# Performance work log

Measured on AMD Instinct MI355X. Metric: run time of the kernel, lower is better.

## Reference

```python
import jax, jax.numpy as jnp
import numpy as np


def setup_inputs() -> dict:
    key = jax.random.key(0)
    ks = jax.random.split(key, 6)
    Q, S, D, C = 128, 512, 768, 64
    return {
        "query_reps": jax.random.normal(ks[0], (Q, D), dtype=jnp.float32),
        "support_reps": jax.random.normal(ks[1], (S, D), dtype=jnp.float32),
        "W1": jax.random.normal(ks[2], (2 * D, 2 * D), dtype=jnp.float32) * 0.02,
        "b1": jnp.zeros((2 * D,), dtype=jnp.float32),
        "W2": jax.random.normal(ks[3], (1, 2 * D), dtype=jnp.float32) * 0.02,
        "b2": jnp.zeros((1,), dtype=jnp.float32),
        "support_labels": jnp.sort(jax.random.randint(ks[4], (S,), 0, C)),
        "query_target_ids": jax.random.randint(ks[5], (Q,), 0, C),
        "num_classes": C,
    }


def reference(query_reps, support_reps, W1, b1, W2, b2,
              support_labels, query_target_ids, num_classes):
    D = query_reps.shape[1]
    # Original: concat_reps = cat([repeat_interleave(q, S), s.repeat(Q)], dim=1)
    # then relu(Linear_2Dx2D(concat)). Equivalent split-weight form avoids the
    # explicit [Q*S, 2D] concat: x @ W1.T = q @ W1[:, :D].T + s @ W1[:, D:].T
    hq = query_reps @ W1[:, :D].T        # [Q, 2D]
    hs = support_reps @ W1[:, D:].T      # [S, 2D]
    h = jax.nn.relu(hq[:, None, :] + hs[None, :, :] + b1)   # [Q, S, 2D]
    scores = jnp.einsum('qsd,d->qs', h, W2[0]) + b2[0]       # [Q, S]
    # aggregate_scores_by_label with support_reduction='score':
    # M one-hot [C, S] row-normalized (p=1) => per-label mean of scores.
    seg = jax.ops.segment_sum(scores.T, support_labels,
                              num_segments=num_classes).T     # [Q, C]
    counts = jax.ops.segment_sum(jnp.ones((support_labels.shape[0],), jnp.float32),
                                 support_labels, num_segments=num_classes)
    agg = seg / jnp.maximum(counts, 1.0)                      # [Q, C]
    logp = jax.nn.log_softmax(agg, axis=1)
    loss = -jnp.mean(jnp.take_along_axis(logp, query_target_ids[:, None], axis=1))
    preds = jnp.argmax(agg, axis=1)
    return (loss, preds == query_target_ids)
```

## Files before the change

kernel.cpp:

```cpp
#include <hip/hip_runtime.h>
#include <math.h>

#define QN 128
#define SN 512
#define DN 768
#define TDN 1536
#define CN 64
#define KSPLIT 2
#define KCH 384

#define HQP_ELEMS (KSPLIT * QN * TDN)
#define HSP_ELEMS (KSPLIT * SN * TDN)
#define ZERO_ELEMS (QN * CN)

typedef short short8 __attribute__((ext_vector_type(8)));
typedef float f32x4 __attribute__((ext_vector_type(4)));

#define LDS_STRIDE 40
#define PLANE (128 * LDS_STRIDE)

__device__ __forceinline__ short bf16_rtn(float x) {
    unsigned u = __float_as_uint(x);
    return (short)((u + 0x7fffu + ((u >> 16) & 1u)) >> 16);
}
__device__ __forceinline__ float bf16_tof(short s) {
    return __uint_as_float(((unsigned)(unsigned short)s) << 16);
}

__global__ __launch_bounds__(256) void gemm_kernel(
    const float* __restrict__ query, const float* __restrict__ support,
    const float* __restrict__ W1, float* __restrict__ hqp, float* __restrict__ hsp,
    float* __restrict__ zbuf, int* __restrict__ donecnt)
{
    const int nt = blockIdx.x;
    const int mt = blockIdx.y;
    const int kz = blockIdx.z;
    const int tid = threadIdx.x;

    if (nt == 0 && kz == 0) {
        int o = (mt * 256 + tid) * 8;
        if (o < ZERO_ELEMS) {
            *(float4*)&zbuf[o]     = make_float4(0.f, 0.f, 0.f, 0.f);
            *(float4*)&zbuf[o + 4] = make_float4(0.f, 0.f, 0.f, 0.f);
        }
        if (mt == 0 && tid == 0) *donecnt = 0;
    }

    const float* A;
    float* Cout;
    int M0, Koff;
    if (mt == 0) { A = query;   M0 = 0;              Koff = 0;  Cout = hqp + (size_t)kz * QN * TDN; }
    else         { A = support; M0 = (mt - 1) * 128; Koff = DN; Cout = hsp + (size_t)kz * SN * TDN; }

    __shared__ short lds[2][4][PLANE];

    const int r  = tid >> 1;
    const int kh = (tid & 1) * 16;

    const float* Arow = &A [(size_t)(M0 + r) * DN  + kz * KCH + kh];
    const float* Brow = &W1[(size_t)(nt * 128 + r) * TDN + Koff + kz * KCH + kh];

    f32x4 acc[4][4];
    #pragma unroll
    for (int i = 0; i < 4; ++i)
        #pragma unroll
        for (int j = 0; j < 4; ++j)
            acc[i][j] = (f32x4){0.f, 0.f, 0.f, 0.f};

    auto stage = [&](short* plane, float4 v0, float4 v1, float4 v2, float4 v3) {
        float f[16] = {v0.x,v0.y,v0.z,v0.w, v1.x,v1.y,v1.z,v1.w,
                       v2.x,v2.y,v2.z,v2.w, v3.x,v3.y,v3.z,v3.w};
        short hi[16], lo[16];
        #pragma unroll
        for (int i = 0; i < 16; ++i) {
            hi[i] = bf16_rtn(f[i]);
            lo[i] = bf16_rtn(f[i] - bf16_tof(hi[i]));
        }
        short* dsth = plane + r * LDS_STRIDE + kh;
        #pragma unroll
        for (int i = 0; i < 16; ++i) dsth[i] = hi[i];
        short* dstl = plane + PLANE + r * LDS_STRIDE + kh;
        #pragma unroll
        for (int i = 0; i < 16; ++i) dstl[i] = lo[i];
    };

    {
        float4 a0 = *(const float4*)(Arow),     a1 = *(const float4*)(Arow + 4);
        float4 a2 = *(const float4*)(Arow + 8), a3 = *(const float4*)(Arow + 12);
        float4 b0 = *(const float4*)(Brow),     b1 = *(const float4*)(Brow + 4);
        float4 b2 = *(const float4*)(Brow + 8), b3 = *(const float4*)(Brow + 12);
        stage(lds[0][0], a0, a1, a2, a3);
        stage(lds[0][2], b0, b1, b2, b3);
    }
    __syncthreads();

    const int lane  = tid & 63;
    const int w     = tid >> 6;
    const int lm    = lane & 15;
    const int quad  = lane >> 4;
    const int wrow0 = (w >> 1) * 64;
    const int wcol0 = (w & 1) * 64;

    int buf = 0;
    for (int step = 0; step < 12; ++step) {
        float4 a0, a1, a2, a3, b0, b1, b2, b3;
        if (step < 11) {
            const float* An = Arow + (step + 1) * 32;
            const float* Bn = Brow + (step + 1) * 32;
            a0 = *(const float4*)(An);     a1 = *(const float4*)(An + 4);
            a2 = *(const float4*)(An + 8); a3 = *(const float4*)(An + 12);
            b0 = *(const float4*)(Bn);     b1 = *(const float4*)(Bn + 4);
            b2 = *(const float4*)(Bn + 8); b3 = *(const float4*)(Bn + 12);
        }

        const short* Ah = lds[buf][0];
        const short* Al = lds[buf][1];
        const short* Bh = lds[buf][2];
        const short* Bl = lds[buf][3];

        short8 ah[4], al[4], bh[4], bl[4];
        #pragma unroll
        for (int mi = 0; mi < 4; ++mi) {
            int off = (wrow0 + mi * 16 + lm) * LDS_STRIDE + quad * 8;
            ah[mi] = *(const short8*)&Ah[off];
            al[mi] = *(const short8*)&Al[off];
        }
        #pragma unroll
        for (int ni = 0; ni < 4; ++ni) {
            int off = (wcol0 + ni * 16 + lm) * LDS_STRIDE + quad * 8;
            bh[ni] = *(const short8*)&Bh[off];
            bl[ni] = *(const short8*)&Bl[off];
        }
        #pragma unroll
        for (int mi = 0; mi < 4; ++mi)
            #pragma unroll
            for (int ni = 0; ni < 4; ++ni) {
                acc[mi][ni] = __builtin_amdgcn_mfma_f32_16x16x32_bf16(ah[mi], bh[ni], acc[mi][ni], 0, 0, 0);
                acc[mi][ni] = __builtin_amdgcn_mfma_f32_16x16x32_bf16(ah[mi], bl[ni], acc[mi][ni], 0, 0, 0);
                acc[mi][ni] = __builtin_amdgcn_mfma_f32_16x16x32_bf16(al[mi], bh[ni], acc[mi][ni], 0, 0, 0);
            }

        if (step < 11) {
            int nb = buf ^ 1;
            stage(lds[nb][0], a0, a1, a2, a3);
            stage(lds[nb][2], b0, b1, b2, b3);
            __syncthreads();
            buf = nb;
        }
    }

    #pragma unroll
    for (int mi = 0; mi < 4; ++mi)
        #pragma unroll
        for (int ni = 0; ni < 4; ++ni) {
            int grow = M0 + wrow0 + mi * 16 + quad * 4;
            int gcol = nt * 128 + wcol0 + ni * 16 + lm;
            #pragma unroll
            for (int rr = 0; rr < 4; ++rr)
                Cout[(size_t)(grow + rr) * TDN + gcol] = acc[mi][ni][rr];
        }
}

__global__ __launch_bounds__(256) void score_kernel(
    const float* __restrict__ hqp, const float* __restrict__ hsp,
    const float* __restrict__ b1, const float* __restrict__ W2,
    const int* __restrict__ labels, const int* __restrict__ tgt,
    float* __restrict__ aggbuf, int* __restrict__ donecnt,
    float* __restrict__ out)
{
    const int jc = blockIdx.x;
    const int qt = blockIdx.y;
    const int st = blockIdx.z;

    __shared__ float hqT[96][64];
    __shared__ float hsT[96][64];
    __shared__ float w2s[96];
    __shared__ float sc[64][68];
    __shared__ int   lab[64];
    __shared__ float cnt[CN];
    __shared__ float red[2];
    __shared__ int   isLast;

    const int tid = threadIdx.x;
    if (tid < 64) lab[tid] = labels[st * 64 + tid];

    #pragma unroll
    for (int l = 0; l < 6; ++l) {
        int idx  = tid + l * 256;
        int row  = idx / 24;
        int quad = idx - row * 24;
        int j    = jc * 96 + quad * 4;
        float4 hv = *(const float4*)&b1[j];
        float4 sv = make_float4(0.f, 0.f, 0.f, 0.f);
        #pragma unroll
        for (int p = 0; p < KSPLIT; ++p) {
            float4 h = *(const float4*)&hqp[(size_t)p * QN * TDN + (size_t)(qt * 64 + row) * TDN + j];
            float4 g = *(const float4*)&hsp[(size_t)p * SN * TDN + (size_t)(st * 64 + row) * TDN + j];
            hv.x += h.x; hv.y += h.y; hv.z += h.z; hv.w += h.w;
            sv.x += g.x; sv.y += g.y; sv.z += g.z; sv.w += g.w;
        }
        hqT[quad*4+0][row] = hv.x; hqT[quad*4+1][row] = hv.y;
        hqT[quad*4+2][row] = hv.z; hqT[quad*4+3][row] = hv.w;
        hsT[quad*4+0][row] = sv.x; hsT[quad*4+1][row] = sv.y;
        hsT[quad*4+2][row] = sv.z; hsT[quad*4+3][row] = sv.w;
    }
    if (tid < 24) {
        float4 wv = *(const float4*)&W2[jc * 96 + tid * 4];
        w2s[tid*4+0] = wv.x; w2s[tid*4+1] = wv.y;
        w2s[tid*4+2] = wv.z; w2s[tid*4+3] = wv.w;
    }
    __syncthreads();

    const int tx = tid & 15;
    const int ty = tid >> 4;
    float acc[4][4];
    #pragma unroll
    for (int i = 0; i < 4; ++i)
        #pragma unroll
        for (int j = 0; j < 4; ++j) acc[i][j] = 0.0f;

    #pragma unroll 4
    for (int jj = 0; jj < 96; ++jj) {
        float4 a4 = *(const float4*)&hqT[jj][ty * 4];
        float4 b4 = *(const float4*)&hsT[jj][tx * 4];
        float wv = w2s[jj];
        float a[4] = {a4.x, a4.y, a4.z, a4.w};
        float b[4] = {b4.x, b4.y, b4.z, b4.w};
        #pragma unroll
        for (int i = 0; i < 4; ++i)
            #pragma unroll
            for (int j = 0; j < 4; ++j)
                acc[i][j] += wv * fmaxf(a[i] + b[j], 0.0f);
    }

    #pragma unroll
    for (int i = 0; i < 4; ++i)
        *(float4*)&sc[ty * 4 + i][tx * 4] =
            make_float4(acc[i][0], acc[i][1], acc[i][2], acc[i][3]);
    __syncthreads();

    {
        int row = tid >> 2;
        int seg = tid & 3;
        float* aggrow = aggbuf + (size_t)(qt * 64 + row) * CN;
        int   runc = lab[seg * 16];
        float runv = 0.0f;
        #pragma unroll
        for (int k = 0; k < 16; ++k) {
            int s = seg * 16 + k;
            int c = lab[s];
            if (c != runc) { atomicAdd(&aggrow[runc], runv); runv = 0.0f; runc = c; }
            runv += sc[row][s];
        }
        atomicAdd(&aggrow[runc], runv);
    }

    __syncthreads();
    if (tid == 0) {
        __threadfence();
        isLast = (atomicAdd(donecnt, 1) == 255);
    }
    __syncthreads();
    if (!isLast) return;
    __threadfence();

    if (tid < CN) cnt[tid] = 0.0f;
    __syncthreads();
    atomicAdd(&cnt[labels[tid]],       1.0f);
    atomicAdd(&cnt[labels[tid + 256]], 1.0f);
    __syncthreads();

    float lossv = 0.0f;
    if (tid < QN) {
        const int q = tid;
        const float* rowp = aggbuf + (size_t)q * CN;
        const int t = tgt[q];
        float best = -1e30f, vt = 0.0f;
        int bi = 0;
        #pragma unroll
        for (int c = 0; c < CN; ++c) {
            float v = __hip_atomic_load(&rowp[c], __ATOMIC_RELAXED,
                                        __HIP_MEMORY_SCOPE_AGENT)
                      / fmaxf(cnt[c], 1.0f);
            if (v > best) { best = v; bi = c; }
            if (c == t) vt = v;
        }
        float e = 0.0f;
        #pragma unroll
        for (int c = 0; c < CN; ++c) {
            float v = __hip_atomic_load(&rowp[c], __ATOMIC_RELAXED,
                                        __HIP_MEMORY_SCOPE_AGENT)
                      / fmaxf(cnt[c], 1.0f);
            e += expf(v - best);
        }
        out[1 + q] = (bi == t) ? 1.0f : 0.0f;
        lossv = -(vt - best - logf(e));
    }
    #pragma unroll
    for (int off = 1; off < 64; off <<= 1)
        lossv += __shfl_xor(lossv, off);
    if ((tid & 63) == 0) red[tid >> 6] = lossv;
    __syncthreads();
    if (tid == 0) out[0] = (red[0] + red[1]) / (float)QN;
}

extern "C" void kernel_launch(void* const* d_in, const int* in_sizes, int n_in,
                              void* d_out, int out_size, void* d_ws, size_t ws_size,
                              hipStream_t stream) {
    const float* query   = (const float*)d_in[0];
    const float* support = (const float*)d_in[1];
    const float* W1      = (const float*)d_in[2];
    const float* b1      = (const float*)d_in[3];
    const float* W2      = (const float*)d_in[4];
    const int* labels = (const int*)d_in[6];
    const int* tgt    = (const int*)d_in[7];

    float* ws      = (float*)d_ws;
    float* hqp     = ws;
    float* hsp     = hqp + HQP_ELEMS;
    float* aggbuf  = hsp + HSP_ELEMS;
    int*   donecnt = (int*)(aggbuf + QN * CN);
    float* out     = (float*)d_out;

    hipLaunchKernelGGL(gemm_kernel, dim3(12, 5, 2), dim3(256), 0, stream,
                       query, support, W1, hqp, hsp, aggbuf, donecnt);
    hipLaunchKernelGGL(score_kernel, dim3(16, 2, 8), dim3(256), 0, stream,
                       hqp, hsp, b1, W2, labels, tgt, aggbuf, donecnt, out);
}
```

Measured before the change: 143.6 us.

## Halve score-kernel D chunk, swizzle LDS row-major tiles, atomics from registers

The score kernel's hidden-dimension chunk drops from 96 to 48, doubling the grid to 512 blocks to raise parallelism across CUs. Staged hq/hs tiles are now stored row-major with an XOR swizzle and read as float4 per row, replacing the transposed scalar LDS stores. The score tile no longer goes through shared memory: each thread does the label-run segmented atomicAdds directly from its register accumulators. The trade-off is more global atomics, since each thread now issues at least one per row per block, plus twice the blocks contending on the completion counter.

```diff
diff --git a/kernel.cpp b/kernel.cpp
--- a/kernel.cpp
+++ b/kernel.cpp
@@ -161,6 +161,9 @@
         }
 }
 
+#define JC 48
+#define SSTR 68
+
 __global__ __launch_bounds__(256) void score_kernel(
     const float* __restrict__ hqp, const float* __restrict__ hsp,
     const float* __restrict__ b1, const float* __restrict__ W2,
@@ -172,10 +175,9 @@
     const int qt = blockIdx.y;
     const int st = blockIdx.z;
 
-    __shared__ float hqT[96][64];
-    __shared__ float hsT[96][64];
-    __shared__ float w2s[96];
-    __shared__ float sc[64][68];
+    __shared__ float hqL[64 * SSTR];
+    __shared__ float hsL[64 * SSTR];
+    __shared__ float w2s[JC];
     __shared__ int   lab[64];
     __shared__ float cnt[CN];
     __shared__ float red[2];
@@ -183,31 +185,30 @@
 
     const int tid = threadIdx.x;
     if (tid < 64) lab[tid] = labels[st * 64 + tid];
+    if (tid < 12) *(float4*)&w2s[tid * 4] = *(const float4*)&W2[jc * JC + tid * 4];
 
     #pragma unroll
     for (int l = 0; l < 6; ++l) {
         int idx  = tid + l * 256;
-        int row  = idx / 24;
-        int quad = idx - row * 24;
-        int j    = jc * 96 + quad * 4;
-        float4 hv = *(const float4*)&b1[j];
-        float4 sv = make_float4(0.f, 0.f, 0.f, 0.f);
-        #pragma unroll
-        for (int p = 0; p < KSPLIT; ++p) {
-            float4 h = *(const float4*)&hqp[(size_t)p * QN * TDN + (size_t)(qt * 64 + row) * TDN + j];
-            float4 g = *(const float4*)&hsp[(size_t)p * SN * TDN + (size_t)(st * 64 + row) * TDN + j];
-            hv.x += h.x; hv.y += h.y; hv.z += h.z; hv.w += h.w;
-            sv.x += g.x; sv.y += g.y; sv.z += g.z; sv.w += g.w;
-        }
-        hqT[quad*4+0][row] = hv.x; hqT[quad*4+1][row] = hv.y;
-        hqT[quad*4+2][row] = hv.z; hqT[quad*4+3][row] = hv.w;
-        hsT[quad*4+0][row] = sv.x; hsT[quad*4+1][row] = sv.y;
-        hsT[quad*4+2][row] = sv.z; hsT[quad*4+3][row] = sv.w;
-    }
-    if (tid < 24) {
-        float4 wv = *(const float4*)&W2[jc * 96 + tid * 4];
-        w2s[tid*4+0] = wv.x; w2s[tid*4+1] = wv.y;
-        w2s[tid*4+2] = wv.z; w2s[tid*4+3] = wv.w;
+        int isHS = idx >= 768;
+        int slot = isHS ? idx - 768 : idx;
+        int row  = slot / 12;
+        int q4   = slot - row * 12;
+        int j    = jc * JC + q4 * 4;
+        int phys = q4 ^ ((row >> 2) & 7);
+        if (!isHS) {
+            float4 h0 = *(const float4*)&hqp[(size_t)(qt * 64 + row) * TDN + j];
+            float4 h1 = *(const float4*)&hqp[(size_t)QN * TDN + (size_t)(qt * 64 + row) * TDN + j];
+            float4 bb = *(const float4*)&b1[j];
+            *(float4*)&hqL[row * SSTR + phys * 4] =
+                make_float4(h0.x + h1.x + bb.x, h0.y + h1.y + bb.y,
+                            h0.z + h1.z + bb.z, h0.w + h1.w + bb.w);
+        } else {
+            float4 g0 = *(const float4*)&hsp[(size_t)(st * 64 + row) * TDN + j];
+            float4 g1 = *(const float4*)&hsp[(size_t)SN * TDN + (size_t)(st * 64 + row) * TDN + j];
+            *(float4*)&hsL[row * SSTR + phys * 4] =
+                make_float4(g0.x + g1.x, g0.y + g1.y, g0.z + g1.z, g0.w + g1.w);
+        }
     }
     __syncthreads();
 
@@ -219,46 +220,62 @@
         #pragma unroll
         for (int j = 0; j < 4; ++j) acc[i][j] = 0.0f;
 
-    #pragma unroll 4
-    for (int jj = 0; jj < 96; ++jj) {
-        float4 a4 = *(const float4*)&hqT[jj][ty * 4];
-        float4 b4 = *(const float4*)&hsT[jj][tx * 4];
-        float wv = w2s[jj];
-        float a[4] = {a4.x, a4.y, a4.z, a4.w};
-        float b[4] = {b4.x, b4.y, b4.z, b4.w};
+    const int akey = ty & 7;
+    const int bkey = tx & 7;
+
+    for (int jj4 = 0; jj4 < 12; ++jj4) {
+        float4 a4[4], b4[4];
+        const int pa = (jj4 ^ akey) * 4;
+        const int pb = (jj4 ^ bkey) * 4;
         #pragma unroll
         for (int i = 0; i < 4; ++i)
+            a4[i] = *(const float4*)&hqL[(ty * 4 + i) * SSTR + pa];
+        #pragma unroll
+        for (int j = 0; j < 4; ++j)
+            b4[j] = *(const float4*)&hsL[(tx * 4 + j) * SSTR + pb];
+        float4 w4 = *(const float4*)&w2s[jj4 * 4];
+
+        #pragma unroll
+        for (int c = 0; c < 4; ++c) {
+            float w = (c == 0) ? w4.x : (c == 1) ? w4.y : (c == 2) ? w4.z : w4.w;
+            float a[4] = { (c==0)?a4[0].x:(c==1)?a4[0].y:(c==2)?a4[0].z:a4[0].w,
+                           (c==0)?a4[1].x:(c==1)?a4[1].y:(c==2)?a4[1].z:a4[1].w,
+                           (c==0)?a4[2].x:(c==1)?a4[2].y:(c==2)?a4[2].z:a4[2].w,
+                           (c==0)?a4[3].x:(c==1)?a4[3].y:(c==2)?a4[3].z:a4[3].w };
+            float b[4] = { (c==0)?b4[0].x:(c==1)?b4[0].y:(c==2)?b4[0].z:b4[0].w,
+                           (c==0)?b4[1].x:(c==1)?b4[1].y:(c==2)?b4[1].z:b4[1].w,
+                           (c==0)?b4[2].x:(c==1)?b4[2].y:(c==2)?b4[2].z:b4[2].w,
+                           (c==0)?b4[3].x:(c==1)?b4[3].y:(c==2)?b4[3].z:b4[3].w };
             #pragma unroll
-            for (int j = 0; j < 4; ++j)
-                acc[i][j] += wv * fmaxf(a[i] + b[j], 0.0f);
-    }
-
-    #pragma unroll
-    for (int i = 0; i < 4; ++i)
-        *(float4*)&sc[ty * 4 + i][tx * 4] =
-            make_float4(acc[i][0], acc[i][1], acc[i][2], acc[i][3]);
-    __syncthreads();
+            for (int i = 0; i < 4; ++i)
+                #pragma unroll
+                for (int j = 0; j < 4; ++j)
+                    acc[i][j] += w * fmaxf(a[i] + b[j], 0.0f);
+        }
+    }
 
     {
-        int row = tid >> 2;
-        int seg = tid & 3;
-        float* aggrow = aggbuf + (size_t)(qt * 64 + row) * CN;
-        int   runc = lab[seg * 16];
-        float runv = 0.0f;
-        #pragma unroll
-        for (int k = 0; k < 16; ++k) {
-            int s = seg * 16 + k;
-            int c = lab[s];
-            if (c != runc) { atomicAdd(&aggrow[runc], runv); runv = 0.0f; runc = c; }
-            runv += sc[row][s];
-        }
-        atomicAdd(&aggrow[runc], runv);
+        const int l0 = lab[tx * 4 + 0], l1 = lab[tx * 4 + 1];
+        const int l2 = lab[tx * 4 + 2], l3 = lab[tx * 4 + 3];
+        #pragma unroll
+        for (int i = 0; i < 4; ++i) {
+            float* aggrow = aggbuf + (size_t)(qt * 64 + ty * 4 + i) * CN;
+            float runv = acc[i][0];
+            int   runc = l0;
+            if (l1 != runc) { atomicAdd(&aggrow[runc], runv); runv = 0.0f; runc = l1; }
+            runv += acc[i][1];
+            if (l2 != runc) { atomicAdd(&aggrow[runc], runv); runv = 0.0f; runc = l2; }
+            runv += acc[i][2];
+            if (l3 != runc) { atomicAdd(&aggrow[runc], runv); runv = 0.0f; runc = l3; }
+            runv += acc[i][3];
+            atomicAdd(&aggrow[runc], runv);
+        }
     }
 
     __syncthreads();
     if (tid == 0) {
         __threadfence();
-        isLast = (atomicAdd(donecnt, 1) == 255);
+        isLast = (atomicAdd(donecnt, 1) == 511);
     }
     __syncthreads();
     if (!isLast) return;
@@ -324,6 +341,6 @@
 
     hipLaunchKernelGGL(gemm_kernel, dim3(12, 5, 2), dim3(256), 0, stream,
                        query, support, W1, hqp, hsp, aggbuf, donecnt);
-    hipLaunchKernelGGL(score_kernel, dim3(16, 2, 8), dim3(256), 0, stream,
+    hipLaunchKernelGGL(score_kernel, dim3(32, 2, 8), dim3(256), 0, stream,
                        hqp, hsp, b1, W2, labels, tgt, aggbuf, donecnt, out);
 }
```

Measured after the change: 153.3 us. 6.8% more time.
